# Kernel optimization log

Measured on AMD Instinct MI355X. Metric: run time of the kernel, lower is better.

## Reference

```python
import jax, jax.numpy as jnp
import numpy as np

N = 50000
E = 800000
IN_CH = 256
ADIM = 64
EDIM = 16
NUM_CLUSTERS = 8


def setup_inputs() -> dict:
    key = jax.random.key(0)
    ks = jax.random.split(key, 16)
    def lin(k, fan_in, fan_out):
        w = jax.random.normal(k, (fan_in, fan_out), jnp.float32) * (fan_in ** -0.5)
        b = jnp.zeros((fan_out,), jnp.float32)
        return w, b
    W_down, b_down = lin(ks[0], IN_CH, ADIM)
    W_up, b_up = lin(ks[1], ADIM, IN_CH)
    W_time, b_time = lin(ks[2], EDIM, ADIM)
    Wq, bq = lin(ks[3], ADIM, ADIM)
    Wk, bk = lin(ks[4], ADIM, ADIM)
    Wv, bv = lin(ks[5], ADIM, ADIM)
    W_out, b_out = lin(ks[6], ADIM, ADIM)
    cluster_emb = jax.random.normal(ks[7], (NUM_CLUSTERS, ADIM), jnp.float32)
    x = jax.random.normal(ks[8], (N, IN_CH), jnp.float32)
    edge_attr = jax.random.normal(ks[9], (E, EDIM), jnp.float32)
    edge_index = jax.random.randint(ks[10], (2, E), 0, N, jnp.int32)
    return {"x": x, "edge_attr": edge_attr, "edge_index": edge_index,
            "W_down": W_down, "b_down": b_down, "W_up": W_up, "b_up": b_up,
            "W_time": W_time, "b_time": b_time, "Wq": Wq, "bq": bq,
            "Wk": Wk, "bk": bk, "Wv": Wv, "bv": bv,
            "cluster_emb": cluster_emb, "W_out": W_out, "b_out": b_out}


def reference(x, edge_attr, edge_index, W_down, b_down, W_up, b_up,
              W_time, b_time, Wq, bq, Wk, bk, Wv, bv, cluster_emb, W_out, b_out):
    n_nodes = x.shape[0]
    scaling = ADIM ** -0.5

    node_feat = jax.nn.relu(x @ W_down + b_down)              # [N, D]
    time_feat = jax.nn.relu(edge_attr @ W_time + b_time)      # [E, D]

    q = node_feat @ Wq + bq                                   # [N, D]
    k = time_feat @ Wk + bk                                   # [E, D]
    v = time_feat @ Wv + bv                                   # [E, D]

    # cluster assignment: argmax of softmax(sim) == argmax of sim
    sims = (time_feat @ cluster_emb.T) * scaling              # [E, C]
    cluster = jnp.argmax(sims, axis=-1).astype(jnp.int32)     # [E]

    src = edge_index[0]                                       # [E]
    q_i = q[src]                                              # [E, D]
    attn = jnp.sum(q_i * k, axis=-1) * scaling                # [E]

    # per-(cluster, src) segments replicate the per-cluster loop exactly
    seg = cluster * n_nodes + src                             # [E]
    num_seg = NUM_CLUSTERS * n_nodes

    # scatter_softmax within each (cluster, src) group (numerically stable)
    m = jax.ops.segment_max(attn, seg, num_segments=num_seg)
    ex = jnp.exp(attn - m[seg])
    denom = jax.ops.segment_sum(ex, seg, num_segments=num_seg)
    w = ex / denom[seg]                                       # [E]

    wv = v * w[:, None]                                       # [E, D]
    sums = jax.ops.segment_sum(wv, seg, num_segments=num_seg)
    sums = sums.reshape(NUM_CLUSTERS, n_nodes, ADIM)
    counts = jax.ops.segment_sum(jnp.ones((E,), jnp.float32), seg, num_segments=num_seg)
    counts = counts.reshape(NUM_CLUSTERS, n_nodes)
    mean = sums / jnp.maximum(counts, 1.0)[..., None]         # scatter_mean (0 where empty)

    # divide by number of non-empty clusters (len(outputs) in torch loop)
    edges_per_cluster = jax.ops.segment_sum(jnp.ones((E,), jnp.float32), cluster,
                                            num_segments=NUM_CLUSTERS)
    n_nonempty = jnp.sum((edges_per_cluster > 0).astype(jnp.float32))
    combined = jnp.sum(mean, axis=0) / n_nonempty             # [N, D]

    fused = jax.nn.relu(combined @ W_out + b_out)             # [N, D]
    out = x + (fused @ W_up + b_up)                           # [N, in_ch]
    return out
```

## Files before the change

### kernel.cpp

```cpp
#include <hip/hip_runtime.h>

#define NN 50000
#define EE 800000
#define INCH 256
#define D 64
#define ED 16
#define NC 8
#define NB 196
#define NEGINF (-3.0e38f)

__device__ __align__(16) char g_ws[64u << 20];

__device__ __forceinline__ unsigned short f2b(float f){
  unsigned u = __float_as_uint(f);
  return (unsigned short)((u + 0x7fffu + ((u >> 16) & 1u)) >> 16);
}
__device__ __forceinline__ unsigned packbf(float lo, float hi){
  return (unsigned)f2b(lo) | ((unsigned)f2b(hi) << 16);
}
__device__ __forceinline__ float blo(unsigned w){ return __uint_as_float(w << 16); }
__device__ __forceinline__ float bhi(unsigned w){ return __uint_as_float(w & 0xffff0000u); }

__global__ __launch_bounds__(256) void Adapter_30872224923942_kernel(
    unsigned* __restrict__ ws, int nwords)
{
  int stride = gridDim.x * 256;
  for (int i = blockIdx.x * 256 + threadIdx.x; i < nwords; i += stride)
    ws[i] = 0u;
}

__global__ __launch_bounds__(256) void kpre(
    const float* __restrict__ Wq, const float* __restrict__ bq,
    const float* __restrict__ Wk, const float* __restrict__ bk,
    const float* __restrict__ Wv, const float* __restrict__ bv,
    const float* __restrict__ Wo, const float* __restrict__ Wd,
    const float* __restrict__ Wu,
    float* __restrict__ M, float* __restrict__ cvec, float* __restrict__ u,
    float* __restrict__ s0, float* __restrict__ Wvo, float* __restrict__ bvo,
    unsigned* __restrict__ WdP, unsigned* __restrict__ WuP)
{
  int b = blockIdx.x, t = threadIdx.x;
  if (b < 16){
    int i = b*4 + (t >> 6), j = t & 63;
    float acc = 0.0f;
    for (int d = 0; d < D; ++d) acc = fmaf(Wq[i*D+d], Wk[j*D+d], acc);
    M[i*D+j] = acc;
  } else if (b < 32){
    int i = (b-16)*4 + (t >> 6), j = t & 63;
    float acc = 0.0f;
    for (int d = 0; d < D; ++d) acc = fmaf(Wv[i*D+d], Wo[d*D+j], acc);
    Wvo[i*D+j] = acc;
  } else if (b < 36){
    for (int k = 0; k < 8; ++k){
      int idx = (b-32)*2048 + t*8 + k;
      int c2 = idx >> 6, j = idx & 63;
      WdP[idx] = packbf(Wd[(2*c2)*D + j], Wd[(2*c2+1)*D + j]);
    }
  } else if (b < 40){
    for (int k = 0; k < 8; ++k){
      int idx = (b-36)*2048 + t*8 + k;
      int d2 = idx >> 8, c = idx & 255;
      WuP[idx] = packbf(Wu[(2*d2)*INCH + c], Wu[(2*d2+1)*INCH + c]);
    }
  } else {
    if (t < 64){
      float acc = 0.0f;
      for (int d = 0; d < D; ++d) acc = fmaf(Wk[t*D+d], bq[d], acc);
      cvec[t] = acc;
    } else if (t < 128){
      int i = t - 64; float acc = 0.0f;
      for (int d = 0; d < D; ++d) acc = fmaf(Wq[i*D+d], bk[d], acc);
      u[i] = acc;
    } else if (t < 192){
      int j = t - 128; float acc = 0.0f;
      for (int d = 0; d < D; ++d) acc = fmaf(bv[d], Wo[d*D+j], acc);
      bvo[j] = acc;
    } else if (t == 192){
      float acc = 0.0f;
      for (int d = 0; d < D; ++d) acc = fmaf(bq[d], bk[d], acc);
      s0[0] = acc;
    }
  }
}

__global__ __launch_bounds__(256) void p1_hist(
    const int* __restrict__ eidx, int* __restrict__ cnt)
{
  int e = blockIdx.x * 256 + threadIdx.x;
  if (e < EE) atomicAdd(&cnt[eidx[e]], 1);
}

__global__ __launch_bounds__(256) void s1_scan(
    const int* __restrict__ cnt, int* __restrict__ rowptr, int* __restrict__ bsum)
{
  __shared__ int s[256];
  int t = threadIdx.x;
  int i = blockIdx.x * 256 + t;
  int v = (i < NN) ? cnt[i] : 0;
  s[t] = v; __syncthreads();
  #pragma unroll
  for (int off = 1; off < 256; off <<= 1){
    int add = (t >= off) ? s[t - off] : 0;
    __syncthreads();
    s[t] += add;
    __syncthreads();
  }
  if (i < NN) rowptr[i] = s[t] - v;
  if (t == 255) bsum[blockIdx.x] = s[255];
}
__global__ __launch_bounds__(256) void s2_scan(int* __restrict__ bsum)
{
  __shared__ int s[256];
  int t = threadIdx.x;
  int v = (t < NB) ? bsum[t] : 0;
  s[t] = v; __syncthreads();
  #pragma unroll
  for (int off = 1; off < 256; off <<= 1){
    int add = (t >= off) ? s[t - off] : 0;
    __syncthreads();
    s[t] += add;
    __syncthreads();
  }
  if (t < NB) bsum[t] = s[t] - v;
}
__global__ __launch_bounds__(256) void s3_add(
    int* __restrict__ rowptr, const int* __restrict__ bsum)
{
  int i = blockIdx.x * 256 + threadIdx.x;
  if (i < NN) rowptr[i] += bsum[blockIdx.x];
  if (i == 0) rowptr[NN] = EE;
}

__global__ __launch_bounds__(256) void p2_build(
    const int* __restrict__ eidx, const int* __restrict__ rowptr,
    int* __restrict__ fill, int2* __restrict__ pairS)
{
  int e = blockIdx.x * 256 + threadIdx.x;
  if (e >= EE) return;
  int src = eidx[e];
  int r = atomicAdd(&fill[src], 1);
  int2 pr; pr.x = e; pr.y = src;
  pairS[rowptr[src] + r] = pr;
}

__global__ __launch_bounds__(256) void k1_node(
    const float* __restrict__ x, const unsigned* __restrict__ WdP,
    const float* __restrict__ bd, const float* __restrict__ M,
    const float* __restrict__ cvec, const float* __restrict__ u,
    const float* __restrict__ s0p,
    unsigned short* __restrict__ qkH, float* __restrict__ qb)
{
  __shared__ unsigned sWdP[8192];
  __shared__ float sX[16][256];
  __shared__ float sNf[16][64];
  int t = threadIdx.x;
  int lane = t & 63;
  int wg = __builtin_amdgcn_readfirstlane(t >> 6);
  int n0 = blockIdx.x * 16 + wg * 4;
  #pragma unroll
  for (int r = 0; r < 4; ++r){
    const float* gsrc = x + (size_t)(n0 + r) * INCH + lane * 4;
    __builtin_amdgcn_global_load_lds(
        (const __attribute__((address_space(1))) void*)gsrc,
        (__attribute__((address_space(3))) void*)&sX[wg*4 + r][0],
        16, 0, 0);
  }
  #pragma unroll
  for (int i = 0; i < 8; ++i)
    ((uint4*)sWdP)[t + 256*i] = ((const uint4*)WdP)[t + 256*i];
  __syncthreads();
  const float4* xr0 = (const float4*)&sX[wg*4 + 0][0];
  const float4* xr1 = (const float4*)&sX[wg*4 + 1][0];
  const float4* xr2 = (const float4*)&sX[wg*4 + 2][0];
  const float4* xr3 = (const float4*)&sX[wg*4 + 3][0];
  float bdl = bd[lane];
  float a0 = bdl, a1 = bdl, a2 = bdl, a3 = bdl;
  #pragma unroll 4
  for (int c4 = 0; c4 < 64; ++c4){
    float4 x0 = xr0[c4], x1 = xr1[c4], x2 = xr2[c4], x3 = xr3[c4];
    unsigned wA = sWdP[(c4*2  )*64 + lane];
    unsigned wB = sWdP[(c4*2+1)*64 + lane];
    float w0 = blo(wA), w1 = bhi(wA), w2 = blo(wB), w3 = bhi(wB);
    a0 = fmaf(x0.x,w0,a0); a0 = fmaf(x0.y,w1,a0); a0 = fmaf(x0.z,w2,a0); a0 = fmaf(x0.w,w3,a0);
    a1 = fmaf(x1.x,w0,a1); a1 = fmaf(x1.y,w1,a1); a1 = fmaf(x1.z,w2,a1); a1 = fmaf(x1.w,w3,a1);
    a2 = fmaf(x2.x,w0,a2); a2 = fmaf(x2.y,w1,a2); a2 = fmaf(x2.z,w2,a2); a2 = fmaf(x2.w,w3,a2);
    a3 = fmaf(x3.x,w0,a3); a3 = fmaf(x3.y,w1,a3); a3 = fmaf(x3.z,w2,a3); a3 = fmaf(x3.w,w3,a3);
  }
  float n0f = fmaxf(a0, 0.0f), n1f = fmaxf(a1, 0.0f);
  float n2f = fmaxf(a2, 0.0f), n3f = fmaxf(a3, 0.0f);
  sNf[wg*4+0][lane] = n0f;
  sNf[wg*4+1][lane] = n1f;
  sNf[wg*4+2][lane] = n2f;
  sNf[wg*4+3][lane] = n3f;
  float cvl = cvec[lane];
  float q0 = cvl, q1 = cvl, q2 = cvl, q3 = cvl;
  const float4* f0 = (const float4*)&sNf[wg*4+0][0];
  const float4* f1 = (const float4*)&sNf[wg*4+1][0];
  const float4* f2 = (const float4*)&sNf[wg*4+2][0];
  const float4* f3 = (const float4*)&sNf[wg*4+3][0];
  #pragma unroll 4
  for (int i4 = 0; i4 < 16; ++i4){
    float4 v0 = f0[i4], v1 = f1[i4], v2 = f2[i4], v3 = f3[i4];
    float m0 = M[(4*i4+0)*64 + lane];
    float m1 = M[(4*i4+1)*64 + lane];
    float m2 = M[(4*i4+2)*64 + lane];
    float m3 = M[(4*i4+3)*64 + lane];
    q0 = fmaf(v0.x,m0,q0); q0 = fmaf(v0.y,m1,q0); q0 = fmaf(v0.z,m2,q0); q0 = fmaf(v0.w,m3,q0);
    q1 = fmaf(v1.x,m0,q1); q1 = fmaf(v1.y,m1,q1); q1 = fmaf(v1.z,m2,q1); q1 = fmaf(v1.w,m3,q1);
    q2 = fmaf(v2.x,m0,q2); q2 = fmaf(v2.y,m1,q2); q2 = fmaf(v2.z,m2,q2); q2 = fmaf(v2.w,m3,q2);
    q3 = fmaf(v3.x,m0,q3); q3 = fmaf(v3.y,m1,q3); q3 = fmaf(v3.z,m2,q3); q3 = fmaf(v3.w,m3,q3);
  }
  qkH[(size_t)(n0+0)*D + lane] = f2b(q0);
  qkH[(size_t)(n0+1)*D + lane] = f2b(q1);
  qkH[(size_t)(n0+2)*D + lane] = f2b(q2);
  qkH[(size_t)(n0+3)*D + lane] = f2b(q3);
  float ul = u[lane], s00 = s0p[0];
  float b0 = n0f*ul, b1 = n1f*ul, b2 = n2f*ul, b3 = n3f*ul;
  #pragma unroll
  for (int s = 32; s; s >>= 1){
    b0 += __shfl_xor(b0, s); b1 += __shfl_xor(b1, s);
    b2 += __shfl_xor(b2, s); b3 += __shfl_xor(b3, s);
  }
  if (lane == 0){
    qb[n0+0] = b0 + s00; qb[n0+1] = b1 + s00;
    qb[n0+2] = b2 + s00; qb[n0+3] = b3 + s00;
  }
}

__global__ __launch_bounds__(256) void p3_edge(
    const float* __restrict__ ea, const int2* __restrict__ pairS,
    const float* __restrict__ Wt, const float* __restrict__ bt, const float* __restrict__ ce,
    const unsigned short* __restrict__ qkH, const float* __restrict__ qb,
    float* __restrict__ attnS, unsigned char* __restrict__ clS,
    unsigned* __restrict__ epc)
{
  __shared__ float sWt[ED*D];
  __shared__ float sbt[D];
  __shared__ float sce[NC*D];
  __shared__ unsigned s_epc[NC];
  int t = threadIdx.x;
  if (t < NC) s_epc[t] = 0u;
  if (t < ED*D/4)  ((float4*)sWt)[t] = ((const float4*)Wt)[t];
  if (t < D/4)     ((float4*)sbt)[t] = ((const float4*)bt)[t];
  if (t < NC*D/4)  ((float4*)sce)[t] = ((const float4*)ce)[t];
  __syncthreads();
  int pos0 = blockIdx.x * 512 + t;
  int pos1 = pos0 + 256;
  bool v1 = (pos1 < EE);
  int pos1c = v1 ? pos1 : pos0;
  int2 pr0 = pairS[pos0];
  int2 pr1 = pairS[pos1c];
  int e0 = pr0.x, sA = pr0.y;
  int e1 = pr1.x, sB = pr1.y;
  const float4* pa = (const float4*)(ea + (size_t)e0 * ED);
  float4 A0 = pa[0], A1 = pa[1], A2 = pa[2], A3 = pa[3];
  float qb0 = qb[sA];
  const float4* pb = (const float4*)(ea + (size_t)e1 * ED);
  float4 B0 = pb[0], B1 = pb[1], B2 = pb[2], B3 = pb[3];
  float qb1 = qb[sB];
  uint4 Q0[2], Q1[2];
  uint4 QA[8], QB[8];
  {
    const uint4* qp = (const uint4*)(qkH + (size_t)sA * D);
    #pragma unroll
    for (int i = 0; i < 8; ++i) QA[i] = qp[i];
  }
  {
    const uint4* qp = (const uint4*)(qkH + (size_t)sB * D);
    #pragma unroll
    for (int i = 0; i < 8; ++i) QB[i] = qp[i];
  }
  (void)Q0; (void)Q1;
  const float4* sWt4 = (const float4*)sWt;
  const float4* sbt4 = (const float4*)sbt;
  const float4* c4p  = (const float4*)sce;

  {
    float eav[ED] = {A0.x,A0.y,A0.z,A0.w, A1.x,A1.y,A1.z,A1.w,
                     A2.x,A2.y,A2.z,A2.w, A3.x,A3.y,A3.z,A3.w};
    float sims[NC];
    #pragma unroll
    for (int c = 0; c < NC; ++c) sims[c] = 0.0f;
    float at = qb0;
    #pragma unroll
    for (int d4 = 0; d4 < D/4; ++d4){
      float4 acc = sbt4[d4];
      #pragma unroll
      for (int j = 0; j < ED; ++j){
        float4 wv = sWt4[j*(D/4) + d4];
        acc.x = fmaf(eav[j], wv.x, acc.x);
        acc.y = fmaf(eav[j], wv.y, acc.y);
        acc.z = fmaf(eav[j], wv.z, acc.z);
        acc.w = fmaf(eav[j], wv.w, acc.w);
      }
      float t0 = fmaxf(acc.x, 0.0f), t1 = fmaxf(acc.y, 0.0f);
      float t2 = fmaxf(acc.z, 0.0f), t3 = fmaxf(acc.w, 0.0f);
      #pragma unroll
      for (int c = 0; c < NC; ++c){
        float4 cv = c4p[c*(D/4) + d4];
        sims[c] = fmaf(t0, cv.x, sims[c]);
        sims[c] = fmaf(t1, cv.y, sims[c]);
        sims[c] = fmaf(t2, cv.z, sims[c]);
        sims[c] = fmaf(t3, cv.w, sims[c]);
      }
      uint4 qv = QA[d4 >> 1];
      unsigned w0 = (d4 & 1) ? qv.z : qv.x;
      unsigned w1 = (d4 & 1) ? qv.w : qv.y;
      at = fmaf(blo(w0), t0, at);
      at = fmaf(bhi(w0), t1, at);
      at = fmaf(blo(w1), t2, at);
      at = fmaf(bhi(w1), t3, at);
    }
    float best = NEGINF; int bc = 0;
    #pragma unroll
    for (int c = 0; c < NC; ++c){
      if (sims[c] > best){ best = sims[c]; bc = c; }
    }
    at *= 0.125f;
    attnS[pos0] = at;
    clS[pos0] = (unsigned char)bc;
    atomicAdd(&s_epc[bc], 1u);
  }

  if (v1){
    float eav[ED] = {B0.x,B0.y,B0.z,B0.w, B1.x,B1.y,B1.z,B1.w,
                     B2.x,B2.y,B2.z,B2.w, B3.x,B3.y,B3.z,B3.w};
    float sims[NC];
    #pragma unroll
    for (int c = 0; c < NC; ++c) sims[c] = 0.0f;
    float at = qb1;
    #pragma unroll
    for (int d4 = 0; d4 < D/4; ++d4){
      float4 acc = sbt4[d4];
      #pragma unroll
      for (int j = 0; j < ED; ++j){
        float4 wv = sWt4[j*(D/4) + d4];
        acc.x = fmaf(eav[j], wv.x, acc.x);
        acc.y = fmaf(eav[j], wv.y, acc.y);
        acc.z = fmaf(eav[j], wv.z, acc.z);
        acc.w = fmaf(eav[j], wv.w, acc.w);
      }
      float t0 = fmaxf(acc.x, 0.0f), t1 = fmaxf(acc.y, 0.0f);
      float t2 = fmaxf(acc.z, 0.0f), t3 = fmaxf(acc.w, 0.0f);
      #pragma unroll
      for (int c = 0; c < NC; ++c){
        float4 cv = c4p[c*(D/4) + d4];
        sims[c] = fmaf(t0, cv.x, sims[c]);
        sims[c] = fmaf(t1, cv.y, sims[c]);
        sims[c] = fmaf(t2, cv.z, sims[c]);
        sims[c] = fmaf(t3, cv.w, sims[c]);
      }
      uint4 qv = QB[d4 >> 1];
      unsigned w0 = (d4 & 1) ? qv.z : qv.x;
      unsigned w1 = (d4 & 1) ? qv.w : qv.y;
      at = fmaf(blo(w0), t0, at);
      at = fmaf(bhi(w0), t1, at);
      at = fmaf(blo(w1), t2, at);
      at = fmaf(bhi(w1), t3, at);
    }
    float best = NEGINF; int bc = 0;
    #pragma unroll
    for (int c = 0; c < NC; ++c){
      if (sims[c] > best){ best = sims[c]; bc = c; }
    }
    at *= 0.125f;
    attnS[pos1] = at;
    clS[pos1] = (unsigned char)bc;
    atomicAdd(&s_epc[bc], 1u);
  }

  __syncthreads();
  if (t < NC){
    unsigned v = s_epc[t];
    if (v) atomicAdd(&epc[t], v);
  }
}

#define EROW 20
__global__ __launch_bounds__(256) void p4_node(
    const float* __restrict__ ea, const int2* __restrict__ pairS,
    const float* __restrict__ Wt, const float* __restrict__ bt,
    const float* __restrict__ attnS, const unsigned char* __restrict__ clS,
    const int* __restrict__ rowptr,
    float* __restrict__ T, float* __restrict__ S)
{
  __shared__ float s_den[4][NC];
  __shared__ int   s_cnt[4][NC];
  __shared__ float s_inv[4][NC];
  __shared__ float s_coef[4][64];
  __shared__ float s_ea[4][64][EROW];
  int t = threadIdx.x, lane = t & 63, w = t >> 6;
  float wl[ED];
  #pragma unroll
  for (int j = 0; j < ED; ++j) wl[j] = Wt[j*D + lane];
  float btl = bt[lane];
  if (lane < NC){ s_den[w][lane] = 0.0f; s_cnt[w][lane] = 0; }
  int node = blockIdx.x * 4 + w;
  int start = rowptr[node], end = rowptr[node + 1];
  for (int base = start; base < end; base += 64){
    int idx = base + lane;
    if (idx < end){
      float ex = __expf(attnS[idx]);
      int c = clS[idx];
      atomicAdd(&s_den[w][c], ex);
      atomicAdd(&s_cnt[w][c], 1);
    }
  }
  if (lane < NC){
    int   cc = s_cnt[w][lane];
    float dd = s_den[w][lane];
    s_inv[w][lane] = (cc > 0) ? 1.0f / (dd * (float)cc) : 0.0f;
    float sv = (cc > 0) ? 1.0f / (float)cc : 0.0f;
    sv += __shfl_xor(sv, 1); sv += __shfl_xor(sv, 2); sv += __shfl_xor(sv, 4);
    if (lane == 0) S[node] = sv;
  }
  float Tacc = 0.0f;
  for (int base = start; base < end; base += 64){
    int idx = base + lane;
    if (idx < end)
      s_coef[w][lane] = __expf(attnS[idx]) * s_inv[w][clS[idx]];
    #pragma unroll
    for (int r = 0; r < 4; ++r){
      int slot = base + r*16 + (lane >> 2);
      if (slot < end){
        int e = pairS[slot].x;
        float4 v = ((const float4*)ea)[(size_t)e*4 + (lane & 3)];
        *(float4*)&s_ea[w][slot - base][(lane & 3)*4] = v;
      }
    }
    int mm = min(64, end - base);
    for (int tt = 0; tt < mm; ++tt){
      float coef = s_coef[w][tt];
      const float4* er = (const float4*)&s_ea[w][tt][0];
      float4 e0 = er[0], e1 = er[1], e2 = er[2], e3 = er[3];
      float tfv = btl;
      tfv = fmaf(e0.x, wl[0], tfv);  tfv = fmaf(e0.y, wl[1], tfv);
      tfv = fmaf(e0.z, wl[2], tfv);  tfv = fmaf(e0.w, wl[3], tfv);
      tfv = fmaf(e1.x, wl[4], tfv);  tfv = fmaf(e1.y, wl[5], tfv);
      tfv = fmaf(e1.z, wl[6], tfv);  tfv = fmaf(e1.w, wl[7], tfv);
      tfv = fmaf(e2.x, wl[8], tfv);  tfv = fmaf(e2.y, wl[9], tfv);
      tfv = fmaf(e2.z, wl[10], tfv); tfv = fmaf(e2.w, wl[11], tfv);
      tfv = fmaf(e3.x, wl[12], tfv); tfv = fmaf(e3.y, wl[13], tfv);
      tfv = fmaf(e3.z, wl[14], tfv); tfv = fmaf(e3.w, wl[15], tfv);
      tfv = fmaxf(tfv, 0.0f);
      Tacc = fmaf(coef, tfv, Tacc);
    }
  }
  T[(size_t)node * D + lane] = Tacc;
}

__global__ __launch_bounds__(256) void k5_out(
    const float* __restrict__ x, const float* __restrict__ T, const float* __restrict__ S,
    const float* __restrict__ Wvo, const float* __restrict__ bvo,
    const unsigned* __restrict__ WuP, const float* __restrict__ bu,
    const float* __restrict__ bo, const unsigned* __restrict__ epc,
    float* __restrict__ out)
{
  __shared__ unsigned sWuP[8192];
  __shared__ float s_fu[16*64];
  int t = threadIdx.x;
  #pragma unroll
  for (int i = 0; i < 8; ++i)
    ((uint4*)sWuP)[t + 256*i] = ((const uint4*)WuP)[t + 256*i];
  int lane = t & 63;
  int wg = __builtin_amdgcn_readfirstlane(t >> 6);
  int n0 = blockIdx.x * 16 + wg * 4;
  float nne = 0.0f;
  #pragma unroll
  for (int c = 0; c < NC; ++c) nne += (epc[c] > 0u) ? 1.0f : 0.0f;
  float inv = 1.0f / fmaxf(nne, 1.0f);
  float T0 = T[(size_t)(n0+0)*D + lane];
  float T1 = T[(size_t)(n0+1)*D + lane];
  float T2 = T[(size_t)(n0+2)*D + lane];
  float T3 = T[(size_t)(n0+3)*D + lane];
  float bvl = bvo[lane], bol = bo[lane];
  float f0 = S[n0+0]*bvl, f1 = S[n0+1]*bvl, f2 = S[n0+2]*bvl, f3 = S[n0+3]*bvl;
  #pragma unroll 8
  for (int i = 0; i < 64; ++i){
    float wv = Wvo[i*64 + lane];
    f0 = fmaf(__shfl(T0, i), wv, f0);
    f1 = fmaf(__shfl(T1, i), wv, f1);
    f2 = fmaf(__shfl(T2, i), wv, f2);
    f3 = fmaf(__shfl(T3, i), wv, f3);
  }
  f0 = fmaxf(f0*inv + bol, 0.0f);
  f1 = fmaxf(f1*inv + bol, 0.0f);
  f2 = fmaxf(f2*inv + bol, 0.0f);
  f3 = fmaxf(f3*inv + bol, 0.0f);
  s_fu[(wg*4+0)*64 + lane] = f0;
  s_fu[(wg*4+1)*64 + lane] = f1;
  s_fu[(wg*4+2)*64 + lane] = f2;
  s_fu[(wg*4+3)*64 + lane] = f3;
  __syncthreads();
  float4 bu4 = ((const float4*)bu)[lane];
  float4 o0 = ((const float4*)(x + (size_t)(n0+0)*INCH))[lane];
  float4 o1 = ((const float4*)(x + (size_t)(n0+1)*INCH))[lane];
  float4 o2 = ((const float4*)(x + (size_t)(n0+2)*INCH))[lane];
  float4 o3 = ((const float4*)(x + (size_t)(n0+3)*INCH))[lane];
  o0.x += bu4.x; o0.y += bu4.y; o0.z += bu4.z; o0.w += bu4.w;
  o1.x += bu4.x; o1.y += bu4.y; o1.z += bu4.z; o1.w += bu4.w;
  o2.x += bu4.x; o2.y += bu4.y; o2.z += bu4.z; o2.w += bu4.w;
  o3.x += bu4.x; o3.y += bu4.y; o3.z += bu4.z; o3.w += bu4.w;
  const float2* fu2 = (const float2*)s_fu;
  #pragma unroll 4
  for (int d2 = 0; d2 < 32; ++d2){
    uint4 wp = *(const uint4*)&sWuP[d2*256 + lane*4];
    float4 wlv = { blo(wp.x), blo(wp.y), blo(wp.z), blo(wp.w) };
    float4 wh  = { bhi(wp.x), bhi(wp.y), bhi(wp.z), bhi(wp.w) };
    float2 g0 = fu2[(wg*4+0)*32 + d2];
    float2 g1 = fu2[(wg*4+1)*32 + d2];
    float2 g2 = fu2[(wg*4+2)*32 + d2];
    float2 g3 = fu2[(wg*4+3)*32 + d2];
    o0.x = fmaf(g0.x, wlv.x, o0.x); o0.y = fmaf(g0.x, wlv.y, o0.y);
    o0.z = fmaf(g0.x, wlv.z, o0.z); o0.w = fmaf(g0.x, wlv.w, o0.w);
    o0.x = fmaf(g0.y, wh.x, o0.x);  o0.y = fmaf(g0.y, wh.y, o0.y);
    o0.z = fmaf(g0.y, wh.z, o0.z);  o0.w = fmaf(g0.y, wh.w, o0.w);
    o1.x = fmaf(g1.x, wlv.x, o1.x); o1.y = fmaf(g1.x, wlv.y, o1.y);
    o1.z = fmaf(g1.x, wlv.z, o1.z); o1.w = fmaf(g1.x, wlv.w, o1.w);
    o1.x = fmaf(g1.y, wh.x, o1.x);  o1.y = fmaf(g1.y, wh.y, o1.y);
    o1.z = fmaf(g1.y, wh.z, o1.z);  o1.w = fmaf(g1.y, wh.w, o1.w);
    o2.x = fmaf(g2.x, wlv.x, o2.x); o2.y = fmaf(g2.x, wlv.y, o2.y);
    o2.z = fmaf(g2.x, wlv.z, o2.z); o2.w = fmaf(g2.x, wlv.w, o2.w);
    o2.x = fmaf(g2.y, wh.x, o2.x);  o2.y = fmaf(g2.y, wh.y, o2.y);
    o2.z = fmaf(g2.y, wh.z, o2.z);  o2.w = fmaf(g2.y, wh.w, o2.w);
    o3.x = fmaf(g3.x, wlv.x, o3.x); o3.y = fmaf(g3.x, wlv.y, o3.y);
    o3.z = fmaf(g3.x, wlv.z, o3.z); o3.w = fmaf(g3.x, wlv.w, o3.w);
    o3.x = fmaf(g3.y, wh.x, o3.x);  o3.y = fmaf(g3.y, wh.y, o3.y);
    o3.z = fmaf(g3.y, wh.z, o3.z);  o3.w = fmaf(g3.y, wh.w, o3.w);
  }
  ((float4*)(out + (size_t)(n0+0)*INCH))[lane] = o0;
  ((float4*)(out + (size_t)(n0+1)*INCH))[lane] = o1;
  ((float4*)(out + (size_t)(n0+2)*INCH))[lane] = o2;
  ((float4*)(out + (size_t)(n0+3)*INCH))[lane] = o3;
}

extern "C" void kernel_launch(void* const* d_in, const int* in_sizes, int n_in,
                              void* d_out, int out_size, void* d_ws, size_t ws_size,
                              hipStream_t stream)
{
  const float* x  = (const float*)d_in[0];
  const float* ea = (const float*)d_in[1];
  const int* eidx = (const int*)d_in[2];
  const float* Wd = (const float*)d_in[3];  const float* bd = (const float*)d_in[4];
  const float* Wu = (const float*)d_in[5];  const float* bu = (const float*)d_in[6];
  const float* Wt = (const float*)d_in[7];  const float* bt = (const float*)d_in[8];
  const float* Wq = (const float*)d_in[9];  const float* bq = (const float*)d_in[10];
  const float* Wk = (const float*)d_in[11]; const float* bk = (const float*)d_in[12];
  const float* Wv = (const float*)d_in[13]; const float* bv = (const float*)d_in[14];
  const float* ce = (const float*)d_in[15];
  const float* Wo = (const float*)d_in[16]; const float* bo = (const float*)d_in[17];
  float* out = (float*)d_out;

  size_t need = 0;
  need += (size_t)NN*4;
  need += (size_t)NN*4;
  need += 64;
  size_t zbytes = need;
  need += (size_t)(NN+4)*4;
  need += 1024;
  need += (size_t)NN*D*2;
  need += (size_t)NN*4;
  need += (size_t)EE*8;
  need += (size_t)EE*4;
  need += (size_t)EE;
  need += (size_t)NN*D*4;
  need += (size_t)NN*4;
  need += 4096*4 + 256 + 256 + 16 + 4096*4 + 256;
  need += 8192*4 + 8192*4;

  char* w = (char*)d_ws;
  if (ws_size < need){
    void* p = nullptr;
    hipGetSymbolAddress(&p, HIP_SYMBOL(g_ws));
    w = (char*)p;
  }
  size_t off = 0;
  int*      cnt    = (int*)(w + off);      off += (size_t)NN*4;
  int*      fill   = (int*)(w + off);      off += (size_t)NN*4;
  unsigned* epc    = (unsigned*)(w + off); off += 64;
  int*      rowptr = (int*)(w + off);      off += (size_t)(NN+4)*4;
  int*      bsum   = (int*)(w + off);      off += 1024;
  unsigned short* qkH = (unsigned short*)(w + off); off += (size_t)NN*D*2;
  float*    qb     = (float*)(w + off);    off += (size_t)NN*4;
  int2*     pairS  = (int2*)(w + off);     off += (size_t)EE*8;
  float*    attnS  = (float*)(w + off);    off += (size_t)EE*4;
  unsigned char* clS = (unsigned char*)(w + off); off += (size_t)EE;
  off = (off + 15) & ~(size_t)15;
  float*    T      = (float*)(w + off);    off += (size_t)NN*D*4;
  float*    S      = (float*)(w + off);    off += (size_t)NN*4;
  float*    M      = (float*)(w + off);    off += 4096*4;
  float*    cvec   = (float*)(w + off);    off += 256;
  float*    u      = (float*)(w + off);    off += 256;
  float*    s0     = (float*)(w + off);    off += 16;
  float*    Wvo    = (float*)(w + off);    off += 4096*4;
  float*    bvo    = (float*)(w + off);    off += 256;
  unsigned* WdP    = (unsigned*)(w + off); off += 8192*4;
  unsigned* WuP    = (unsigned*)(w + off); off += 8192*4;

  int zwords = (int)(zbytes / 4);
  Adapter_30872224923942_kernel<<<dim3(128), dim3(256), 0, stream>>>((unsigned*)w, zwords);
  kpre<<<dim3(41), dim3(256), 0, stream>>>(Wq, bq, Wk, bk, Wv, bv, Wo, Wd, Wu,
                                           M, cvec, u, s0, Wvo, bvo, WdP, WuP);
  p1_hist<<<dim3(EE/256), dim3(256), 0, stream>>>(eidx, cnt);
  s1_scan<<<dim3(NB), dim3(256), 0, stream>>>(cnt, rowptr, bsum);
  s2_scan<<<dim3(1),  dim3(256), 0, stream>>>(bsum);
  s3_add <<<dim3(NB), dim3(256), 0, stream>>>(rowptr, bsum);
  p2_build<<<dim3(EE/256), dim3(256), 0, stream>>>(eidx, rowptr, fill, pairS);
  k1_node<<<dim3(NN/16), dim3(256), 0, stream>>>(x, WdP, bd, M, cvec, u, s0, qkH, qb);
  p3_edge<<<dim3((EE + 511)/512), dim3(256), 0, stream>>>(ea, pairS, Wt, bt, ce, qkH, qb,
                                                          attnS, clS, epc);
  p4_node<<<dim3(NN/4), dim3(256), 0, stream>>>(ea, pairS, Wt, bt, attnS, clS, rowptr, T, S);
  k5_out <<<dim3(NN/16), dim3(256), 0, stream>>>(x, T, S, Wvo, bvo, WuP, bu, bo, epc, out);
}
```

Baseline: 449.1 us.

## Process edges in original order in p3 and read weights from global

```diff
diff --git a/kernel.cpp b/kernel.cpp
--- a/kernel.cpp
+++ b/kernel.cpp
@@ -228,37 +228,28 @@
 }
 
 __global__ __launch_bounds__(256) void p3_edge(
-    const float* __restrict__ ea, const int2* __restrict__ pairS,
+    const float* __restrict__ ea, const int* __restrict__ eidx,
     const float* __restrict__ Wt, const float* __restrict__ bt, const float* __restrict__ ce,
     const unsigned short* __restrict__ qkH, const float* __restrict__ qb,
-    float* __restrict__ attnS, unsigned char* __restrict__ clS,
+    float* __restrict__ attnE, unsigned char* __restrict__ clE,
     unsigned* __restrict__ epc)
 {
-  __shared__ float sWt[ED*D];
-  __shared__ float sbt[D];
-  __shared__ float sce[NC*D];
   __shared__ unsigned s_epc[NC];
   int t = threadIdx.x;
   if (t < NC) s_epc[t] = 0u;
-  if (t < ED*D/4)  ((float4*)sWt)[t] = ((const float4*)Wt)[t];
-  if (t < D/4)     ((float4*)sbt)[t] = ((const float4*)bt)[t];
-  if (t < NC*D/4)  ((float4*)sce)[t] = ((const float4*)ce)[t];
   __syncthreads();
-  int pos0 = blockIdx.x * 512 + t;
-  int pos1 = pos0 + 256;
-  bool v1 = (pos1 < EE);
-  int pos1c = v1 ? pos1 : pos0;
-  int2 pr0 = pairS[pos0];
-  int2 pr1 = pairS[pos1c];
-  int e0 = pr0.x, sA = pr0.y;
-  int e1 = pr1.x, sB = pr1.y;
+  int e0 = blockIdx.x * 512 + t;
+  int e1 = e0 + 256;
+  bool v1 = (e1 < EE);
+  int e1c = v1 ? e1 : e0;
+  int sA = eidx[e0];
+  int sB = eidx[e1c];
   const float4* pa = (const float4*)(ea + (size_t)e0 * ED);
   float4 A0 = pa[0], A1 = pa[1], A2 = pa[2], A3 = pa[3];
   float qb0 = qb[sA];
-  const float4* pb = (const float4*)(ea + (size_t)e1 * ED);
+  const float4* pb = (const float4*)(ea + (size_t)e1c * ED);
   float4 B0 = pb[0], B1 = pb[1], B2 = pb[2], B3 = pb[3];
   float qb1 = qb[sB];
-  uint4 Q0[2], Q1[2];
   uint4 QA[8], QB[8];
   {
     const uint4* qp = (const uint4*)(qkH + (size_t)sA * D);
@@ -270,10 +261,9 @@
     #pragma unroll
     for (int i = 0; i < 8; ++i) QB[i] = qp[i];
   }
-  (void)Q0; (void)Q1;
-  const float4* sWt4 = (const float4*)sWt;
-  const float4* sbt4 = (const float4*)sbt;
-  const float4* c4p  = (const float4*)sce;
+  const float4* Wt4 = (const float4*)Wt;
+  const float4* bt4 = (const float4*)bt;
+  const float4* ce4 = (const float4*)ce;
 
   {
     float eav[ED] = {A0.x,A0.y,A0.z,A0.w, A1.x,A1.y,A1.z,A1.w,
@@ -284,10 +274,10 @@
     float at = qb0;
     #pragma unroll
     for (int d4 = 0; d4 < D/4; ++d4){
-      float4 acc = sbt4[d4];
+      float4 acc = bt4[d4];
       #pragma unroll
       for (int j = 0; j < ED; ++j){
-        float4 wv = sWt4[j*(D/4) + d4];
+        float4 wv = Wt4[j*(D/4) + d4];
         acc.x = fmaf(eav[j], wv.x, acc.x);
         acc.y = fmaf(eav[j], wv.y, acc.y);
         acc.z = fmaf(eav[j], wv.z, acc.z);
@@ -297,7 +287,7 @@
       float t2 = fmaxf(acc.z, 0.0f), t3 = fmaxf(acc.w, 0.0f);
       #pragma unroll
       for (int c = 0; c < NC; ++c){
-        float4 cv = c4p[c*(D/4) + d4];
+        float4 cv = ce4[c*(D/4) + d4];
         sims[c] = fmaf(t0, cv.x, sims[c]);
         sims[c] = fmaf(t1, cv.y, sims[c]);
         sims[c] = fmaf(t2, cv.z, sims[c]);
@@ -317,8 +307,8 @@
       if (sims[c] > best){ best = sims[c]; bc = c; }
     }
     at *= 0.125f;
-    attnS[pos0] = at;
-    clS[pos0] = (unsigned char)bc;
+    attnE[e0] = at;
+    clE[e0] = (unsigned char)bc;
     atomicAdd(&s_epc[bc], 1u);
   }
 
@@ -331,10 +321,10 @@
     float at = qb1;
     #pragma unroll
     for (int d4 = 0; d4 < D/4; ++d4){
-      float4 acc = sbt4[d4];
+      float4 acc = bt4[d4];
       #pragma unroll
       for (int j = 0; j < ED; ++j){
-        float4 wv = sWt4[j*(D/4) + d4];
+        float4 wv = Wt4[j*(D/4) + d4];
         acc.x = fmaf(eav[j], wv.x, acc.x);
         acc.y = fmaf(eav[j], wv.y, acc.y);
         acc.z = fmaf(eav[j], wv.z, acc.z);
@@ -344,7 +334,7 @@
       float t2 = fmaxf(acc.z, 0.0f), t3 = fmaxf(acc.w, 0.0f);
       #pragma unroll
       for (int c = 0; c < NC; ++c){
-        float4 cv = c4p[c*(D/4) + d4];
+        float4 cv = ce4[c*(D/4) + d4];
         sims[c] = fmaf(t0, cv.x, sims[c]);
         sims[c] = fmaf(t1, cv.y, sims[c]);
         sims[c] = fmaf(t2, cv.z, sims[c]);
@@ -364,8 +354,8 @@
       if (sims[c] > best){ best = sims[c]; bc = c; }
     }
     at *= 0.125f;
-    attnS[pos1] = at;
-    clS[pos1] = (unsigned char)bc;
+    attnE[e1] = at;
+    clE[e1] = (unsigned char)bc;
     atomicAdd(&s_epc[bc], 1u);
   }
 
@@ -380,7 +370,7 @@
 __global__ __launch_bounds__(256) void p4_node(
     const float* __restrict__ ea, const int2* __restrict__ pairS,
     const float* __restrict__ Wt, const float* __restrict__ bt,
-    const float* __restrict__ attnS, const unsigned char* __restrict__ clS,
+    const float* __restrict__ attnE, const unsigned char* __restrict__ clE,
     const int* __restrict__ rowptr,
     float* __restrict__ T, float* __restrict__ S)
 {
@@ -400,8 +390,9 @@
   for (int base = start; base < end; base += 64){
     int idx = base + lane;
     if (idx < end){
-      float ex = __expf(attnS[idx]);
-      int c = clS[idx];
+      int e = pairS[idx].x;
+      float ex = __expf(attnE[e]);
+      int c = clE[e];
       atomicAdd(&s_den[w][c], ex);
       atomicAdd(&s_cnt[w][c], 1);
     }
@@ -417,8 +408,10 @@
   float Tacc = 0.0f;
   for (int base = start; base < end; base += 64){
     int idx = base + lane;
-    if (idx < end)
-      s_coef[w][lane] = __expf(attnS[idx]) * s_inv[w][clS[idx]];
+    if (idx < end){
+      int e = pairS[idx].x;
+      s_coef[w][lane] = __expf(attnE[e]) * s_inv[w][clE[e]];
+    }
     #pragma unroll
     for (int r = 0; r < 4; ++r){
       int slot = base + r*16 + (lane >> 2);
@@ -583,8 +576,8 @@
   unsigned short* qkH = (unsigned short*)(w + off); off += (size_t)NN*D*2;
   float*    qb     = (float*)(w + off);    off += (size_t)NN*4;
   int2*     pairS  = (int2*)(w + off);     off += (size_t)EE*8;
-  float*    attnS  = (float*)(w + off);    off += (size_t)EE*4;
-  unsigned char* clS = (unsigned char*)(w + off); off += (size_t)EE;
+  float*    attnE  = (float*)(w + off);    off += (size_t)EE*4;
+  unsigned char* clE = (unsigned char*)(w + off); off += (size_t)EE;
   off = (off + 15) & ~(size_t)15;
   float*    T      = (float*)(w + off);    off += (size_t)NN*D*4;
   float*    S      = (float*)(w + off);    off += (size_t)NN*4;
@@ -607,8 +600,8 @@
   s3_add <<<dim3(NB), dim3(256), 0, stream>>>(rowptr, bsum);
   p2_build<<<dim3(EE/256), dim3(256), 0, stream>>>(eidx, rowptr, fill, pairS);
   k1_node<<<dim3(NN/16), dim3(256), 0, stream>>>(x, WdP, bd, M, cvec, u, s0, qkH, qb);
-  p3_edge<<<dim3((EE + 511)/512), dim3(256), 0, stream>>>(ea, pairS, Wt, bt, ce, qkH, qb,
-                                                          attnS, clS, epc);
-  p4_node<<<dim3(NN/4), dim3(256), 0, stream>>>(ea, pairS, Wt, bt, attnS, clS, rowptr, T, S);
+  p3_edge<<<dim3((EE + 511)/512), dim3(256), 0, stream>>>(ea, eidx, Wt, bt, ce, qkH, qb,
+                                                          attnE, clE, epc);
+  p4_node<<<dim3(NN/4), dim3(256), 0, stream>>>(ea, pairS, Wt, bt, attnE, clE, rowptr, T, S);
   k5_out <<<dim3(NN/16), dim3(256), 0, stream>>>(x, T, S, Wvo, bvo, WuP, bu, bo, epc, out);
 }
```

Measured after the change: 446.2 us. Within noise of the previous version (-0.7%).
